# Kernel tuning notes

Measured on AMD Instinct MI355X. Metric: run time of the kernel, lower is better.

Reference implementation:

```python
import jax, jax.numpy as jnp
import numpy as np

NUM_HEADS = 16
HEAD_DIM = 64
MAX_REL = 128
NEG_INF = -1e30


def setup_inputs() -> dict:
    key = jax.random.key(0)
    ks = jax.random.split(key, 5)
    B, L, D = 2, 2048, 1024
    x = jax.random.normal(ks[0], (B, L, D), dtype=jnp.float32)
    key_padding_mask = jnp.zeros((B, L), dtype=bool)  # True = padded
    Wqkv = jax.random.normal(ks[1], (D, 3 * D), dtype=jnp.float32) * (D ** -0.5)
    bqkv = jnp.zeros((3 * D,), dtype=jnp.float32)
    Wout = jax.random.normal(ks[2], (D, D), dtype=jnp.float32) * (D ** -0.5)
    bout = jnp.zeros((D,), dtype=jnp.float32)
    bias_table = jax.random.normal(ks[3], (2 * MAX_REL + 1, NUM_HEADS), dtype=jnp.float32) * 0.02
    return {"x": x, "key_padding_mask": key_padding_mask, "Wqkv": Wqkv,
            "bqkv": bqkv, "Wout": Wout, "bout": bout, "bias_table": bias_table}


def _rel_bias(bias_table, L):
    # relative position index: clamp(k - q, -MAX_REL, MAX_REL) + MAX_REL -> [L, L]
    rel = jnp.arange(L)[None, :] - jnp.arange(L)[:, None]
    idx = jnp.clip(rel, -MAX_REL, MAX_REL) + MAX_REL
    return bias_table[idx].transpose(2, 0, 1)  # [H, L, L]


def reference(x, key_padding_mask, Wqkv, bqkv, Wout, bout, bias_table):
    B, L, D = x.shape
    H, hd = NUM_HEADS, HEAD_DIM
    qkv = x @ Wqkv + bqkv                      # [B, L, 3D]
    q, k, v = jnp.split(qkv, 3, axis=-1)
    q = q.reshape(B, L, H, hd).transpose(0, 2, 1, 3)  # [B, H, L, hd]
    k = k.reshape(B, L, H, hd).transpose(0, 2, 1, 3)
    v = v.reshape(B, L, H, hd).transpose(0, 2, 1, 3)
    scores = jnp.einsum('bhqd,bhkd->bhqk', q, k) * (hd ** -0.5)
    scores = scores + _rel_bias(bias_table, L)[None]   # [B, H, L, L]
    scores = jnp.where(key_padding_mask[:, None, None, :], NEG_INF, scores)
    attn = jax.nn.softmax(scores, axis=-1)
    out = jnp.einsum('bhqk,bhkd->bhqd', attn, v)       # [B, H, L, hd]
    out = out.transpose(0, 2, 1, 3).reshape(B, L, D)
    return out @ Wout + bout
```

## Files before the change

kernel.cpp:

```cpp
#include <hip/hip_runtime.h>
#include <hip/hip_bf16.h>
#include <stdint.h>

#define LSEQ 2048
#define BATCH 2
#define DMODEL 1024
#define NH 16
#define HD 64

typedef __attribute__((ext_vector_type(8))) short bf16x8;
typedef __attribute__((ext_vector_type(4))) float f32x4;

__device__ __forceinline__ short f2bf(float f) {
  union { float f; uint32_t u; } v; v.f = f;
  uint32_t r = v.u + 0x8000u;
  return (short)(r >> 16);
}

__device__ __forceinline__ uint32_t pack_bf16(float lo, float hi) {
  __hip_bfloat162 hb = __float22bfloat162_rn(float2{lo, hi});
  union { __hip_bfloat162 h; uint32_t u; } cv; cv.h = hb;
  return cv.u;
}

__device__ __forceinline__ float exp2_fast(float x) {
#if __has_builtin(__builtin_amdgcn_exp2f)
  return __builtin_amdgcn_exp2f(x);
#else
  float r; asm("v_exp_f32 %0, %1" : "=v"(r) : "v"(x)); return r;
#endif
}

__device__ __forceinline__ void gll16(const void* g, void* l) {
  __builtin_amdgcn_global_load_lds(
      (const __attribute__((address_space(1))) void*)g,
      (__attribute__((address_space(3))) void*)l, 16, 0, 0);
}

__global__ void prep_kernel(const float* __restrict__ x, const float* __restrict__ Wqkv,
                            const float* __restrict__ Wout, short* __restrict__ xbf,
                            short* __restrict__ wqkvT, short* __restrict__ woutT) {
  __shared__ float tile[32][33];
  const int bid = blockIdx.x;
  if (bid < 4096) {
    int i = (bid * 256 + threadIdx.x) * 4;
    float4 v = *(const float4*)(x + i);
    short4 o;
    o.x = f2bf(v.x); o.y = f2bf(v.y); o.z = f2bf(v.z); o.w = f2bf(v.w);
    *(short4*)(xbf + i) = o;
    return;
  }
  const float* in; short* out; int K, N, t;
  if (bid < 7168) { in = Wqkv; out = wqkvT; K = 1024; N = 3072; t = bid - 4096; }
  else            { in = Wout; out = woutT; K = 1024; N = 1024; t = bid - 7168; }
  int kb = (t & 31) * 32, nb = (t >> 5) * 32;
  int tx = threadIdx.x & 31, ty = threadIdx.x >> 5;
  #pragma unroll
  for (int i = ty; i < 32; i += 8)
    tile[i][tx] = in[(size_t)(kb + i) * N + nb + tx];
  __syncthreads();
  #pragma unroll
  for (int i = ty; i < 32; i += 8)
    out[(size_t)(nb + i) * K + kb + tx] = f2bf(tile[tx][i]);
}

__global__ __launch_bounds__(256, 2) void gemm_qkv(
    const short* __restrict__ A, const short* __restrict__ Bt,
    const float* __restrict__ bias,
    short* __restrict__ q_out, short* __restrict__ k_out, short* __restrict__ v_out) {
  constexpr int K = 1024, BK = 64, NKT = K / BK;
  __shared__ short Als[2][128 * BK];
  __shared__ short Bls[2][128 * BK];
  const int tid = threadIdx.x;
  const int lane = tid & 63;
  const int c = lane & 15, g = lane >> 4;
  const int m0 = blockIdx.x * 128;
  const int n0 = blockIdx.y * 128;
  const int wid = tid >> 6;
  const int wm = (wid >> 1) * 64, wn = (wid & 1) * 64;

  f32x4 acc[4][4] = {};

  auto stage = [&](int kt, int bbuf) {
    const int k0 = kt * BK;
    #pragma unroll
    for (int inst = 0; inst < 4; ++inst) {
      int i = inst * 256 + tid;
      int row = i >> 3, cg = i & 7;
      int scc = cg ^ (row & 7);
      gll16(A + (size_t)(m0 + row) * K + k0 + scc * 8, &Als[bbuf][i * 8]);
      gll16(Bt + (size_t)(n0 + row) * K + k0 + scc * 8, &Bls[bbuf][i * 8]);
    }
  };

  stage(0, 0);

  for (int kt = 0; kt < NKT; ++kt) {
    const int bb = kt & 1;
    asm volatile("s_waitcnt vmcnt(0)" ::: "memory");
    __builtin_amdgcn_s_barrier();
    if (kt < NKT - 1) stage(kt + 1, bb ^ 1);

    #pragma unroll
    for (int ks = 0; ks < 2; ++ks) {
      const int kb = ks * 64 + g * 16;
      bf16x8 af[4], bfv[4];
      #pragma unroll
      for (int m = 0; m < 4; ++m) {
        int row = wm + m * 16 + c;
        af[m] = *(const bf16x8*)((const char*)&Als[bb][0] + row * 128 + (kb ^ ((row & 7) << 4)));
      }
      #pragma unroll
      for (int n = 0; n < 4; ++n) {
        int row = wn + n * 16 + c;
        bfv[n] = *(const bf16x8*)((const char*)&Bls[bb][0] + row * 128 + (kb ^ ((row & 7) << 4)));
      }
      __builtin_amdgcn_s_setprio(1);
      #pragma unroll
      for (int m = 0; m < 4; ++m)
        #pragma unroll
        for (int n = 0; n < 4; ++n)
          acc[m][n] = __builtin_amdgcn_mfma_f32_16x16x32_bf16(af[m], bfv[n], acc[m][n], 0, 0, 0);
      __builtin_amdgcn_s_setprio(0);
    }
  }

  #pragma unroll
  for (int m = 0; m < 4; ++m) {
    #pragma unroll
    for (int n = 0; n < 4; ++n) {
      #pragma unroll
      for (int r = 0; r < 4; ++r) {
        int row = m0 + wm + m * 16 + g * 4 + r;
        int col = n0 + wn + n * 16 + c;
        float val = acc[m][n][r] + bias[col];
        int b = row >> 11, l = row & 2047;
        int which = col >> 10, rem = col & 1023;
        int hn = rem >> 6, d = rem & 63;
        size_t bh = (size_t)b * NH + hn;
        if (which == 0)       q_out[(bh * LSEQ + l) * HD + d] = f2bf(val * 0.1803368801f);
        else if (which == 1)  k_out[(bh * LSEQ + l) * HD + d] = f2bf(val);
        else                  v_out[(bh * HD + d) * LSEQ + l] = f2bf(val);
      }
    }
  }
}

__global__ __launch_bounds__(256, 3) void gemm_out64(
    const short* __restrict__ A, const short* __restrict__ Bt,
    const float* __restrict__ bias, float* __restrict__ outf) {
  constexpr int K = 1024, BK = 64, NKT = K / BK;
  __shared__ short Als[2][128 * BK];
  __shared__ short Bls[2][64 * BK];
  const int tid = threadIdx.x;
  const int lane = tid & 63;
  const int c = lane & 15, g = lane >> 4;
  const int m0 = blockIdx.x * 128;
  const int n0 = blockIdx.y * 64;
  const int wid = tid >> 6;
  const int wm = (wid >> 1) * 64, wn = (wid & 1) * 32;

  f32x4 acc[4][2] = {};

  auto stage = [&](int kt, int bbuf) {
    const int k0 = kt * BK;
    #pragma unroll
    for (int inst = 0; inst < 4; ++inst) {
      int i = inst * 256 + tid;
      int row = i >> 3, cg = i & 7;
      int scc = cg ^ (row & 7);
      gll16(A + (size_t)(m0 + row) * K + k0 + scc * 8, &Als[bbuf][i * 8]);
      if (inst < 2)
        gll16(Bt + (size_t)(n0 + row) * K + k0 + scc * 8, &Bls[bbuf][i * 8]);
    }
  };

  stage(0, 0);

  for (int kt = 0; kt < NKT; ++kt) {
    const int bb = kt & 1;
    asm volatile("s_waitcnt vmcnt(0)" ::: "memory");
    __builtin_amdgcn_s_barrier();
    if (kt < NKT - 1) stage(kt + 1, bb ^ 1);

    #pragma unroll
    for (int ks = 0; ks < 2; ++ks) {
      const int kb = ks * 64 + g * 16;
      bf16x8 af[4], bfv[2];
      #pragma unroll
      for (int m = 0; m < 4; ++m) {
        int row = wm + m * 16 + c;
        af[m] = *(const bf16x8*)((const char*)&Als[bb][0] + row * 128 + (kb ^ ((row & 7) << 4)));
      }
      #pragma unroll
      for (int n = 0; n < 2; ++n) {
        int row = wn + n * 16 + c;
        bfv[n] = *(const bf16x8*)((const char*)&Bls[bb][0] + row * 128 + (kb ^ ((row & 7) << 4)));
      }
      __builtin_amdgcn_s_setprio(1);
      #pragma unroll
      for (int m = 0; m < 4; ++m)
        #pragma unroll
        for (int n = 0; n < 2; ++n)
          acc[m][n] = __builtin_amdgcn_mfma_f32_16x16x32_bf16(af[m], bfv[n], acc[m][n], 0, 0, 0);
      __builtin_amdgcn_s_setprio(0);
    }
  }

  #pragma unroll
  for (int m = 0; m < 4; ++m) {
    #pragma unroll
    for (int n = 0; n < 2; ++n) {
      #pragma unroll
      for (int r = 0; r < 4; ++r) {
        int row = m0 + wm + m * 16 + g * 4 + r;
        int col = n0 + wn + n * 16 + c;
        outf[(size_t)row * DMODEL + col] = acc[m][n][r] + bias[col];
      }
    }
  }
}

__global__ __launch_bounds__(256, 2) void attn_kernel(
    const short* __restrict__ qb, const short* __restrict__ kb,
    const short* __restrict__ vtb, const unsigned char* __restrict__ kpm,
    const float* __restrict__ bias_table, short* __restrict__ ob) {
  constexpr int NT = LSEQ / 64;
  __shared__ short Kls[2][64 * 64];
  __shared__ short Vls[2][64 * 64];
  __shared__ uint2 Pls[4][512];
  __shared__ float biasc[257];
  __shared__ unsigned mbits_s;

  const int tid = threadIdx.x, lane = tid & 63, wid = tid >> 6;
  const int g = lane >> 4, c = lane & 15;
  const int lin = blockIdx.x;
  const int swz = (lin & 7) * 64 + (lin >> 3);
  const int q0 = (swz & 15) * 128;
  const int h = (swz >> 4) & 15;
  const int b = swz >> 8;
  const size_t bh = (size_t)b * NH + h;
  const short* qbase = qb + bh * LSEQ * HD;
  const short* kbase = kb + bh * LSEQ * HD;
  const short* vbase = vtb + bh * HD * LSEQ;
  const unsigned char* kpmb = kpm + (size_t)b * LSEQ;

  bf16x8 qf[2][2];
  #pragma unroll
  for (int qg = 0; qg < 2; ++qg)
    #pragma unroll
    for (int ks = 0; ks < 2; ++ks) {
      int qrow = q0 + wid * 32 + qg * 16 + c;
      qf[qg][ks] = *(const bf16x8*)(qbase + (size_t)qrow * HD + ks * 32 + g * 8);
    }

  if (tid < 32) {
    const uint4* mp = (const uint4*)(kpmb + tid * 64);
    uint4 m0 = mp[0], m1 = mp[1], m2 = mp[2], m3 = mp[3];
    unsigned anyb = m0.x | m0.y | m0.z | m0.w | m1.x | m1.y | m1.z | m1.w |
                    m2.x | m2.y | m2.z | m2.w | m3.x | m3.y | m3.z | m3.w;
    unsigned long long bal = __ballot(anyb != 0);
    if (tid == 0) mbits_s = (unsigned)bal;
  }
  for (int i = tid; i < 257; i += 256) biasc[i] = bias_table[i * NH + h] * 1.44269504f;
  __syncthreads();
  const unsigned mbits = mbits_s;
  const float cb_lo = biasc[0], cb_hi = biasc[256];

  auto stage = [&](int t, int bbuf) {
    const int kv0s = t * 64;
    #pragma unroll
    for (int inst = 0; inst < 2; ++inst) {
      int cc0 = inst * 256 + tid;
      int row = cc0 >> 3, cc = cc0 & 7;
      int scc = cc ^ (row & 7);
      gll16(kbase + (size_t)(kv0s + row) * HD + scc * 8, &Kls[bbuf][cc0 * 8]);
      gll16(vbase + (size_t)row * LSEQ + kv0s + scc * 8, &Vls[bbuf][cc0 * 8]);
    }
  };

  f32x4 o[4][2], l_acc[2];
  #pragma unroll
  for (int nt = 0; nt < 4; ++nt)
    #pragma unroll
    for (int qg = 0; qg < 2; ++qg) o[nt][qg] = (f32x4){0.f, 0.f, 0.f, 0.f};
  l_acc[0] = (f32x4){0.f, 0.f, 0.f, 0.f};
  l_acc[1] = (f32x4){0.f, 0.f, 0.f, 0.f};

  bf16x8 onesf;
  #pragma unroll
  for (int j = 0; j < 8; ++j) onesf[j] = (short)0x3F80;

  uint2* pw = &Pls[wid][0];
  const int c7s = (c & 7) << 4;
  const int cx  = (c & 7) << 1;

  stage(0, 0);

  for (int t = 0; t < NT; ++t) {
    const int bb = t & 1;
    const int kv0 = t * 64;
    asm volatile("s_waitcnt vmcnt(0)" ::: "memory");
    __builtin_amdgcn_s_barrier();
    if (t < NT - 1) stage(t + 1, bb ^ 1);

    f32x4 st[4][2];
    __builtin_amdgcn_s_setprio(1);
    #pragma unroll
    for (int nt = 0; nt < 4; ++nt) {
      f32x4 a0 = {}, a1 = {};
      #pragma unroll
      for (int ks = 0; ks < 2; ++ks) {
        int krow = nt * 16 + c;
        int kbyte = ks * 64 + g * 16;
        const bf16x8 kf =
            *(const bf16x8*)((const char*)&Kls[bb][0] + krow * 128 + (kbyte ^ c7s));
        a0 = __builtin_amdgcn_mfma_f32_16x16x32_bf16(kf, qf[0][ks], a0, 0, 0, 0);
        a1 = __builtin_amdgcn_mfma_f32_16x16x32_bf16(kf, qf[1][ks], a1, 0, 0, 0);
      }
      st[nt][0] = a0; st[nt][1] = a1;
    }
    __builtin_amdgcn_s_setprio(0);

    const int dw = kv0 - q0 - wid * 32;
    if (dw >= 160 || dw <= -192) {
      const float cb = dw > 0 ? cb_hi : cb_lo;
      #pragma unroll
      for (int nt = 0; nt < 4; ++nt)
        #pragma unroll
        for (int qg = 0; qg < 2; ++qg)
          #pragma unroll
          for (int r = 0; r < 4; ++r) st[nt][qg][r] += cb;
    } else {
      #pragma unroll
      for (int nt = 0; nt < 4; ++nt)
        #pragma unroll
        for (int qg = 0; qg < 2; ++qg) {
          const int base = dw + nt * 16 + g * 4 - qg * 16 - c;
          #pragma unroll
          for (int r = 0; r < 4; ++r) {
            int rel = base + r;
            rel = rel < -128 ? -128 : (rel > 128 ? 128 : rel);
            st[nt][qg][r] += biasc[rel + 128];
          }
        }
    }
    if (mbits & (1u << t)) {
      #pragma unroll
      for (int nt = 0; nt < 4; ++nt)
        #pragma unroll
        for (int r = 0; r < 4; ++r) {
          float mk = kpmb[kv0 + nt * 16 + g * 4 + r] ? -1e30f : 0.f;
          st[nt][0][r] += mk;
          st[nt][1][r] += mk;
        }
    }

    #pragma unroll
    for (int qg = 0; qg < 2; ++qg)
      #pragma unroll
      for (int nt = 0; nt < 4; ++nt) {
        uint2 w;
        w.x = pack_bf16(exp2_fast(st[nt][qg][0]), exp2_fast(st[nt][qg][1]));
        w.y = pack_bf16(exp2_fast(st[nt][qg][2]), exp2_fast(st[nt][qg][3]));
        pw[(qg * 16 + c) * 16 + ((nt * 4 + g) ^ cx)] = w;
      }

    #pragma unroll
    for (int ks = 0; ks < 2; ++ks) {
      const int pu = (ks * 8 + g * 2) ^ cx;
      union { uint2 u[2]; bf16x8 v; } pa0u, pa1u;
      pa0u.u[0] = pw[c * 16 + pu];        pa0u.u[1] = pw[c * 16 + pu + 1];
      pa1u.u[0] = pw[(16 + c) * 16 + pu]; pa1u.u[1] = pw[(16 + c) * 16 + pu + 1];
      const bf16x8 pa0 = pa0u.v, pa1 = pa1u.v;
      l_acc[0] = __builtin_amdgcn_mfma_f32_16x16x32_bf16(pa0, onesf, l_acc[0], 0, 0, 0);
      l_acc[1] = __builtin_amdgcn_mfma_f32_16x16x32_bf16(pa1, onesf, l_acc[1], 0, 0, 0);
      const int pbyte = ks * 64 + g * 16;
      #pragma unroll
      for (int nt = 0; nt < 4; ++nt) {
        int vrow = nt * 16 + c;
        const bf16x8 vf =
            *(const bf16x8*)((const char*)&Vls[bb][0] + vrow * 128 + (pbyte ^ c7s));
        o[nt][0] = __builtin_amdgcn_mfma_f32_16x16x32_bf16(pa0, vf, o[nt][0], 0, 0, 0);
        o[nt][1] = __builtin_amdgcn_mfma_f32_16x16x32_bf16(pa1, vf, o[nt][1], 0, 0, 0);
      }
    }
  }

  #pragma unroll
  for (int qg = 0; qg < 2; ++qg)
    #pragma unroll
    for (int r = 0; r < 4; ++r) {
      float inv = 1.f / l_acc[qg][r];
      int qrow = q0 + wid * 32 + qg * 16 + g * 4 + r;
      size_t obase = ((size_t)b * LSEQ + qrow) * DMODEL + (size_t)h * HD;
      #pragma unroll
      for (int nt = 0; nt < 4; ++nt)
        ob[obase + nt * 16 + c] = f2bf(o[nt][qg][r] * inv);
    }
}

extern "C" void kernel_launch(void* const* d_in, const int* in_sizes, int n_in,
                              void* d_out, int out_size, void* d_ws, size_t ws_size,
                              hipStream_t stream) {
  (void)in_sizes; (void)n_in; (void)out_size; (void)ws_size;
  const float* x = (const float*)d_in[0];
  const unsigned char* kpm = (const unsigned char*)d_in[1];
  const float* Wqkv = (const float*)d_in[2];
  const float* bqkv = (const float*)d_in[3];
  const float* Wout = (const float*)d_in[4];
  const float* bout = (const float*)d_in[5];
  const float* btab = (const float*)d_in[6];
  float* out = (float*)d_out;

  short* ws = (short*)d_ws;
  short* xbf   = ws;
  short* wqkvT = xbf + 4194304;
  short* woutT = wqkvT + 3145728;
  short* qbuf  = woutT + 1048576;
  short* kbuf  = qbuf + 4194304;
  short* vtbuf = kbuf + 4194304;
  short* obuf  = vtbuf + 4194304;

  prep_kernel<<<dim3(8192), dim3(256), 0, stream>>>(x, Wqkv, Wout, xbf, wqkvT, woutT);

  gemm_qkv<<<dim3(32, 24), dim3(256), 0, stream>>>(xbf, wqkvT, bqkv,
                                                   qbuf, kbuf, vtbuf);
  attn_kernel<<<dim3(512), dim3(256), 0, stream>>>(qbuf, kbuf, vtbuf, kpm, btab, obuf);
  gemm_out64<<<dim3(32, 16), dim3(256), 0, stream>>>(obuf, woutT, bout, out);
}
```

Measured before the change: 127.2 us.

## Software-pipeline QK^T of next tile with softmax and PV of previous tile

```diff
diff --git a/kernel.cpp b/kernel.cpp
--- a/kernel.cpp
+++ b/kernel.cpp
@@ -267,15 +267,26 @@
   const unsigned mbits = mbits_s;
   const float cb_lo = biasc[0], cb_hi = biasc[256];
 
-  auto stage = [&](int t, int bbuf) {
+  auto stageK = [&](int t, int bbuf) {
     const int kv0s = t * 64;
+    int row = tid >> 2, cc = tid & 3;
+    (void)row; (void)cc;
     #pragma unroll
     for (int inst = 0; inst < 2; ++inst) {
       int cc0 = inst * 256 + tid;
-      int row = cc0 >> 3, cc = cc0 & 7;
-      int scc = cc ^ (row & 7);
-      gll16(kbase + (size_t)(kv0s + row) * HD + scc * 8, &Kls[bbuf][cc0 * 8]);
-      gll16(vbase + (size_t)row * LSEQ + kv0s + scc * 8, &Vls[bbuf][cc0 * 8]);
+      int r2 = cc0 >> 3, cg = cc0 & 7;
+      int scc = cg ^ (r2 & 7);
+      gll16(kbase + (size_t)(kv0s + r2) * HD + scc * 8, &Kls[bbuf][cc0 * 8]);
+    }
+  };
+  auto stageV = [&](int t, int bbuf) {
+    const int kv0s = t * 64;
+    #pragma unroll
+    for (int inst = 0; inst < 2; ++inst) {
+      int cc0 = inst * 256 + tid;
+      int r2 = cc0 >> 3, cg = cc0 & 7;
+      int scc = cg ^ (r2 & 7);
+      gll16(vbase + (size_t)r2 * LSEQ + kv0s + scc * 8, &Vls[bbuf][cc0 * 8]);
     }
   };
 
@@ -295,16 +306,10 @@
   const int c7s = (c & 7) << 4;
   const int cx  = (c & 7) << 1;
 
-  stage(0, 0);
-
-  for (int t = 0; t < NT; ++t) {
-    const int bb = t & 1;
-    const int kv0 = t * 64;
-    asm volatile("s_waitcnt vmcnt(0)" ::: "memory");
-    __builtin_amdgcn_s_barrier();
-    if (t < NT - 1) stage(t + 1, bb ^ 1);
-
-    f32x4 st[4][2];
+  f32x4 st_prev[4][2];
+
+  auto qkt = [&](int t, f32x4 out[4][2]) {
+    const int bbk = t & 1;
     __builtin_amdgcn_s_setprio(1);
     #pragma unroll
     for (int nt = 0; nt < 4; ++nt) {
@@ -314,14 +319,18 @@
         int krow = nt * 16 + c;
         int kbyte = ks * 64 + g * 16;
         const bf16x8 kf =
-            *(const bf16x8*)((const char*)&Kls[bb][0] + krow * 128 + (kbyte ^ c7s));
+            *(const bf16x8*)((const char*)&Kls[bbk][0] + krow * 128 + (kbyte ^ c7s));
         a0 = __builtin_amdgcn_mfma_f32_16x16x32_bf16(kf, qf[0][ks], a0, 0, 0, 0);
         a1 = __builtin_amdgcn_mfma_f32_16x16x32_bf16(kf, qf[1][ks], a1, 0, 0, 0);
       }
-      st[nt][0] = a0; st[nt][1] = a1;
+      out[nt][0] = a0; out[nt][1] = a1;
     }
     __builtin_amdgcn_s_setprio(0);
-
+  };
+
+  auto smpv = [&](int t) {
+    const int kv0 = t * 64;
+    const int bbv = t & 1;
     const int dw = kv0 - q0 - wid * 32;
     if (dw >= 160 || dw <= -192) {
       const float cb = dw > 0 ? cb_hi : cb_lo;
@@ -330,7 +339,7 @@
         #pragma unroll
         for (int qg = 0; qg < 2; ++qg)
           #pragma unroll
-          for (int r = 0; r < 4; ++r) st[nt][qg][r] += cb;
+          for (int r = 0; r < 4; ++r) st_prev[nt][qg][r] += cb;
     } else {
       #pragma unroll
       for (int nt = 0; nt < 4; ++nt)
@@ -341,7 +350,7 @@
           for (int r = 0; r < 4; ++r) {
             int rel = base + r;
             rel = rel < -128 ? -128 : (rel > 128 ? 128 : rel);
-            st[nt][qg][r] += biasc[rel + 128];
+            st_prev[nt][qg][r] += biasc[rel + 128];
           }
         }
     }
@@ -351,8 +360,8 @@
         #pragma unroll
         for (int r = 0; r < 4; ++r) {
           float mk = kpmb[kv0 + nt * 16 + g * 4 + r] ? -1e30f : 0.f;
-          st[nt][0][r] += mk;
-          st[nt][1][r] += mk;
+          st_prev[nt][0][r] += mk;
+          st_prev[nt][1][r] += mk;
         }
     }
 
@@ -361,8 +370,8 @@
       #pragma unroll
       for (int nt = 0; nt < 4; ++nt) {
         uint2 w;
-        w.x = pack_bf16(exp2_fast(st[nt][qg][0]), exp2_fast(st[nt][qg][1]));
-        w.y = pack_bf16(exp2_fast(st[nt][qg][2]), exp2_fast(st[nt][qg][3]));
+        w.x = pack_bf16(exp2_fast(st_prev[nt][qg][0]), exp2_fast(st_prev[nt][qg][1]));
+        w.y = pack_bf16(exp2_fast(st_prev[nt][qg][2]), exp2_fast(st_prev[nt][qg][3]));
         pw[(qg * 16 + c) * 16 + ((nt * 4 + g) ^ cx)] = w;
       }
 
@@ -380,12 +389,35 @@
       for (int nt = 0; nt < 4; ++nt) {
         int vrow = nt * 16 + c;
         const bf16x8 vf =
-            *(const bf16x8*)((const char*)&Vls[bb][0] + vrow * 128 + (pbyte ^ c7s));
+            *(const bf16x8*)((const char*)&Vls[bbv][0] + vrow * 128 + (pbyte ^ c7s));
         o[nt][0] = __builtin_amdgcn_mfma_f32_16x16x32_bf16(pa0, vf, o[nt][0], 0, 0, 0);
         o[nt][1] = __builtin_amdgcn_mfma_f32_16x16x32_bf16(pa1, vf, o[nt][1], 0, 0, 0);
       }
     }
-  }
+  };
+
+  stageK(0, 0);
+
+  for (int t = 0; t < NT; ++t) {
+    asm volatile("s_waitcnt vmcnt(0)" ::: "memory");
+    __builtin_amdgcn_s_barrier();
+    if (t < NT - 1) stageK(t + 1, (t + 1) & 1);
+    stageV(t, t & 1);
+
+    f32x4 st_cur[4][2];
+    qkt(t, st_cur);
+    if (t > 0) smpv(t - 1);
+
+    #pragma unroll
+    for (int nt = 0; nt < 4; ++nt) {
+      st_prev[nt][0] = st_cur[nt][0];
+      st_prev[nt][1] = st_cur[nt][1];
+    }
+  }
+
+  asm volatile("s_waitcnt vmcnt(0)" ::: "memory");
+  __builtin_amdgcn_s_barrier();
+  smpv(NT - 1);
 
   #pragma unroll
   for (int qg = 0; qg < 2; ++qg)
```

New measurement: 128.8 us. Within noise of the previous version (+1.3%).
